# Optimization experiments

Hardware: AMD Instinct MI355X
Metric: run time of the kernel (lower is better)

Reference implementation:

```python
import jax, jax.numpy as jnp
import numpy as np

B, H, W, C, F, K = 64, 56, 56, 256, 256, 3


def _conv(x, w, padding):
    # NHWC input, HWIO kernel, stride 1
    return jax.lax.conv_general_dilated(
        x, w, window_strides=(1, 1), padding=padding,
        dimension_numbers=('NHWC', 'HWIO', 'NHWC'))


def setup_inputs() -> dict:
    key = jax.random.key(0)
    kx, kw = jax.random.split(key)
    x = jax.random.normal(kx, (B, H, W, C), dtype=jnp.float32)
    stdv = 1.0 / np.sqrt(K * K * C)  # matches build()'s init scale
    w = (jax.random.normal(kw, (K, K, C, F), dtype=jnp.float32) * stdv).astype(jnp.float32)
    return {"x": x, "w": w}


def reference(x, w):
    # fp16_grad forward: round-trip weights through fp16
    wq = w.astype(jnp.float16).astype(jnp.float32)
    # binarize_weight forward value: sign(clip(w, -1, 1))
    wb = jnp.sign(jnp.clip(wq, -1.0, 1.0))
    return _conv(x, wb, 'SAME')
```

## Files before the change

kernel.cpp:

```cpp
#include <hip/hip_runtime.h>
#include <hip/hip_bf16.h>
#include <hip/hip_fp16.h>

typedef __bf16 bf16x8 __attribute__((ext_vector_type(8)));
typedef float  f32x4  __attribute__((ext_vector_type(4)));

#define C_H 56
#define C_W 56
#define C_C 256
#define C_F 256
#define C_B 64
#define N_PIX (C_B * C_H * C_W)
#define WB_ELEMS (9 * C_C * C_F)
#define WB_BYTES (WB_ELEMS * 2)
#define ZBUF_BYTES 1024
#define XB_OFF (WB_BYTES + ZBUF_BYTES)
#define X_ELEMS (N_PIX * C_C)

#define GLOAD_LDS16(g, l)                                                   \
    __builtin_amdgcn_global_load_lds(                                        \
        (const __attribute__((address_space(1))) void*)(g),                  \
        (__attribute__((address_space(3))) void*)(l), 16, 0, 0)

__global__ void prep_w_kernel(const float* __restrict__ w, __bf16* __restrict__ wbT) {
    int idx = blockIdx.x * 256 + threadIdx.x;
    int f = idx & 255;
    int c = (idx >> 8) & 255;
    int s = idx >> 16;
    float wf = w[idx];
    float v = __half2float(__float2half(wf));
    float sgn = (v > 0.f) ? 1.f : ((v < 0.f) ? -1.f : 0.f);
    wbT[(s << 16) + (f << 8) + c] = (__bf16)sgn;
}

__global__ void zero_kernel(float* __restrict__ z) {
    z[threadIdx.x] = 0.f;
}

__global__ void prep_x_kernel(const float* __restrict__ x, __bf16* __restrict__ xb) {
    int i = blockIdx.x * 256 + threadIdx.x;
    const f32x4* p = reinterpret_cast<const f32x4*>(x) + (size_t)i * 2;
    f32x4 a = p[0], b = p[1];
    bf16x8 o;
    o[0] = (__bf16)a[0]; o[1] = (__bf16)a[1]; o[2] = (__bf16)a[2]; o[3] = (__bf16)a[3];
    o[4] = (__bf16)b[0]; o[5] = (__bf16)b[1]; o[6] = (__bf16)b[2]; o[7] = (__bf16)b[3];
    reinterpret_cast<bf16x8*>(xb)[i] = o;
}

__global__ __launch_bounds__(512, 2) void conv_mfma8_kernel(
    const char* __restrict__ xbp,
    const char* __restrict__ wbp,
    const char* __restrict__ zp,
    float* __restrict__ out) {

    __shared__ __align__(16) char sm[4][32768];

    const int nbid = (blockIdx.x & 7) * 98 + (blockIdx.x >> 3);
    const long m0 = (long)nbid * 256;

    const int tid  = threadIdx.x;
    const int lane = tid & 63;
    const int wave = tid >> 6;
    const int l15  = lane & 15;
    const int g4   = lane >> 4;
    const int wm   = wave >> 2;
    const int wn   = wave & 3;
    const int colr = ((g4 ^ ((l15 >> 1) & 3)) << 4);
    const int rdA = (wm * 128 + l15) * 64 + colr;
    const int rdB = 16384 + (wn * 64 + l15) * 64 + colr;

    const int r0 = tid >> 2;
    const int sw = ((tid & 3) ^ ((r0 >> 1) & 3)) << 4;
    const int p0 = (int)m0 + r0;
    const int p1 = p0 + 128;
    const int rem0 = p0 % 3136;
    const int rem1 = p1 % 3136;
    const int y0 = rem0 / 56, x0 = rem0 - (rem0 / 56) * 56;
    const int y1 = rem1 / 56, x1 = rem1 - (rem1 / 56) * 56;

    auto stage_half = [&](int kt, int abHalf) {
        int cc = (kt * 57) >> 9;
        int s  = kt - 9 * cc;
        char* L = &sm[kt & 3][0];
        size_t cb = (size_t)(cc << 6) + sw;
        if (abHalf == 0) {
            int s3 = (s * 171) >> 9;
            int dy = s3 - 1;
            int dx = s - 3 * s3 - 1;
            int doff = dy * 56 + dx;
            bool v0 = ((unsigned)(y0 + dy) < 56u) & ((unsigned)(x0 + dx) < 56u);
            bool v1 = ((unsigned)(y1 + dy) < 56u) & ((unsigned)(x1 + dx) < 56u);
            const char* a0 = v0 ? xbp + (size_t)(p0 + doff) * 512 + cb : zp + sw;
            const char* a1 = v1 ? xbp + (size_t)(p1 + doff) * 512 + cb : zp + sw;
            GLOAD_LDS16(a0, L + tid * 16);
            GLOAD_LDS16(a1, L + 8192 + tid * 16);
        } else {
            const char* b0 = wbp + (size_t)((s << 8) + r0) * 512 + cb;
            const char* b1 = wbp + (size_t)((s << 8) + r0 + 128) * 512 + cb;
            GLOAD_LDS16(b0, L + 16384 + tid * 16);
            GLOAD_LDS16(b1, L + 24576 + tid * 16);
        }
    };

    f32x4 acc[8][4];
#pragma unroll
    for (int i = 0; i < 8; ++i)
#pragma unroll
        for (int j = 0; j < 4; ++j)
            acc[i][j] = (f32x4){0.f, 0.f, 0.f, 0.f};

    bf16x8 Af[4], Bf[4];

#define VM8 asm volatile("s_waitcnt vmcnt(8)" ::: "memory")
#define VM4 asm volatile("s_waitcnt vmcnt(4)" ::: "memory")
#define VM0 asm volatile("s_waitcnt vmcnt(0)" ::: "memory")

#define PHASE(Q, H, DOSTAGE, TAILWAIT)                                      \
    {                                                                        \
        const char* Lb = &sm[(Q)][0];                                        \
        if ((H) == 0) {                                                      \
            _Pragma("unroll")                                                \
            for (int bj = 0; bj < 4; ++bj)                                   \
                Bf[bj] = *reinterpret_cast<const bf16x8*>(Lb + rdB + bj * 1024); \
        }                                                                    \
        _Pragma("unroll")                                                    \
        for (int ai = 0; ai < 4; ++ai)                                       \
            Af[ai] = *reinterpret_cast<const bf16x8*>(Lb + rdA + ((H) * 4 + ai) * 1024); \
        if (DOSTAGE) stage_half(kt + 3, (H));                                \
        __builtin_amdgcn_s_barrier();                                        \
        asm volatile("s_waitcnt lgkmcnt(0)" ::: "memory");                   \
        __builtin_amdgcn_sched_barrier(0);                                   \
        __builtin_amdgcn_s_setprio(1);                                       \
        _Pragma("unroll")                                                    \
        for (int ai = 0; ai < 4; ++ai)                                       \
            _Pragma("unroll")                                                \
            for (int bj = 0; bj < 4; ++bj)                                   \
                acc[(H) * 4 + ai][bj] = __builtin_amdgcn_mfma_f32_16x16x32_bf16( \
                    Af[ai], Bf[bj], acc[(H) * 4 + ai][bj], 0, 0, 0);         \
        __builtin_amdgcn_s_setprio(0);                                       \
        __builtin_amdgcn_sched_barrier(0);                                   \
        TAILWAIT;                                                            \
        __builtin_amdgcn_s_barrier();                                        \
    }

    stage_half(0, 0); stage_half(0, 1);
    stage_half(1, 0); stage_half(1, 1);
    stage_half(2, 0); stage_half(2, 1);
    VM8;
    __builtin_amdgcn_s_barrier();

    for (int it = 0; it < 17; ++it) {
        int kt;
        kt = it * 4 + 0; PHASE(0, 0, true, ); PHASE(0, 1, true, VM8);
        kt = it * 4 + 1; PHASE(1, 0, true, ); PHASE(1, 1, true, VM8);
        kt = it * 4 + 2; PHASE(2, 0, true, ); PHASE(2, 1, true, VM8);
        kt = it * 4 + 3; PHASE(3, 0, true, ); PHASE(3, 1, true, VM8);
    }
    { int kt = 68; PHASE(0, 0, true,  ); PHASE(0, 1, true,  VM8); }
    { int kt = 69; PHASE(1, 0, false, ); PHASE(1, 1, false, VM4); }
    { int kt = 70; PHASE(2, 0, false, ); PHASE(2, 1, false, VM0); }
    { int kt = 71; PHASE(3, 0, false, ); PHASE(3, 1, false, ); }

#undef PHASE

#pragma unroll
    for (int ai = 0; ai < 8; ++ai) {
#pragma unroll
        for (int j = 0; j < 4; ++j) {
            long row = m0 + wm * 128 + ai * 16 + g4 * 4 + j;
            float* op = out + row * C_F + wn * 64 + l15;
#pragma unroll
            for (int bj = 0; bj < 4; ++bj)
                op[bj * 16] = acc[ai][bj][j];
        }
    }
}

__global__ __launch_bounds__(256) void conv_fallback_kernel(
    const float* __restrict__ xf,
    const __bf16* __restrict__ wbT, const char* __restrict__ zbuf,
    float* __restrict__ out) {

    const int lane = threadIdx.x & 63;
    const int wave = threadIdx.x >> 6;
    const int l15  = lane & 15;
    const int g    = lane >> 4;
    const int goff = g * 8;
    const long m0  = (long)blockIdx.x * 64;
    const int fbase = wave * 64;

    int ry[4], rx[4];
    long rbase[4];
#pragma unroll
    for (int ai = 0; ai < 4; ++ai) {
        int rr = (int)m0 + ai * 16 + l15;
        int b = rr / 3136;
        int rem = rr - b * 3136;
        int yy2 = rem / 56;
        ry[ai] = yy2;
        rx[ai] = rem - yy2 * 56;
        rbase[ai] = (long)rr * C_C;
    }

    f32x4 acc[4][4];
#pragma unroll
    for (int i = 0; i < 4; ++i)
#pragma unroll
        for (int j = 0; j < 4; ++j)
            acc[i][j] = (f32x4){0.f, 0.f, 0.f, 0.f};

    for (int s = 0; s < 9; ++s) {
        const int dy = s / 3 - 1;
        const int dx = (s - (s / 3) * 3) - 1;
        const float* af[4];
#pragma unroll
        for (int ai = 0; ai < 4; ++ai) {
            bool v = ((unsigned)(ry[ai] + dy) < 56u) & ((unsigned)(rx[ai] + dx) < 56u);
            long off = rbase[ai] + (long)(dy * C_W + dx) * C_C + goff;
            af[ai] = v ? (xf + off) : ((const float*)zbuf + goff);
        }
        const __bf16* bp = wbT + ((size_t)(s * 256 + fbase + l15)) * C_C + goff;

#pragma unroll
        for (int cc = 0; cc < 8; ++cc) {
            const int c0 = cc * 32;
            bf16x8 A[4], Bf[4];
#pragma unroll
            for (int ai = 0; ai < 4; ++ai) {
                const f32x4* p = reinterpret_cast<const f32x4*>(af[ai] + c0);
                f32x4 u = p[0], w2 = p[1];
                bf16x8 t;
                t[0] = (__bf16)u[0]; t[1] = (__bf16)u[1]; t[2] = (__bf16)u[2]; t[3] = (__bf16)u[3];
                t[4] = (__bf16)w2[0]; t[5] = (__bf16)w2[1]; t[6] = (__bf16)w2[2]; t[7] = (__bf16)w2[3];
                A[ai] = t;
            }
#pragma unroll
            for (int bj = 0; bj < 4; ++bj)
                Bf[bj] = *reinterpret_cast<const bf16x8*>(bp + bj * 16 * C_C + c0);
#pragma unroll
            for (int ai = 0; ai < 4; ++ai)
#pragma unroll
                for (int bj = 0; bj < 4; ++bj)
                    acc[ai][bj] = __builtin_amdgcn_mfma_f32_16x16x32_bf16(A[ai], Bf[bj], acc[ai][bj], 0, 0, 0);
        }
    }

#pragma unroll
    for (int ai = 0; ai < 4; ++ai) {
#pragma unroll
        for (int j = 0; j < 4; ++j) {
            long row = m0 + ai * 16 + g * 4 + j;
            float* op = out + row * C_F + fbase + l15;
#pragma unroll
            for (int bj = 0; bj < 4; ++bj)
                op[bj * 16] = acc[ai][bj][j];
        }
    }
}

extern "C" void kernel_launch(void* const* d_in, const int* in_sizes, int n_in,
                              void* d_out, int out_size, void* d_ws, size_t ws_size,
                              hipStream_t stream) {
    const float* x = (const float*)d_in[0];
    const float* w = (const float*)d_in[1];
    float* out = (float*)d_out;

    char* ws = (char*)d_ws;
    __bf16* wbT = (__bf16*)ws;
    char* zbuf = ws + WB_BYTES;
    __bf16* xb = (__bf16*)(ws + XB_OFF);

    const bool prex = ws_size >= (size_t)XB_OFF + (size_t)X_ELEMS * 2;

    prep_w_kernel<<<WB_ELEMS / 256, 256, 0, stream>>>(w, wbT);
    zero_kernel<<<1, 256, 0, stream>>>((float*)zbuf);

    if (prex) {
        prep_x_kernel<<<X_ELEMS / 8 / 256, 256, 0, stream>>>(x, xb);
        conv_mfma8_kernel<<<N_PIX / 256, 512, 0, stream>>>(
            (const char*)xb, (const char*)wbT, zbuf, out);
    } else {
        conv_fallback_kernel<<<N_PIX / 64, 256, 0, stream>>>(x, wbT, zbuf, out);
    }
}
```

Before: 340.7 us.

## Shrink conv tile to 128x128 with 3-stage LDS ring and 256-thread blocks

Replaces the 256x256-tile, 512-thread, 4-buffer MFMA conv kernel with a 128x128 tile (split across M and F tiles), 256 threads, and a 3-deep LDS buffer ring with a single barrier per k-step. The goal is higher occupancy (3 blocks/CU), more blocks for load balance, and simpler synchronisation. The cost is lower arithmetic intensity per block: more global and LDS traffic per FLOP, since x tiles are now loaded twice (once per F half). It also drops the setprio and sched_barrier scheduling hints.

```diff
diff --git a/kernel.cpp b/kernel.cpp
--- a/kernel.cpp
+++ b/kernel.cpp
@@ -47,128 +47,110 @@
     reinterpret_cast<bf16x8*>(xb)[i] = o;
 }
 
-__global__ __launch_bounds__(512, 2) void conv_mfma8_kernel(
+__global__ __launch_bounds__(256, 3) void conv_p3_kernel(
     const char* __restrict__ xbp,
     const char* __restrict__ wbp,
     const char* __restrict__ zp,
     float* __restrict__ out) {
 
-    __shared__ __align__(16) char sm[4][32768];
-
-    const int nbid = (blockIdx.x & 7) * 98 + (blockIdx.x >> 3);
-    const long m0 = (long)nbid * 256;
+    __shared__ __align__(16) char sm[3][16384];
+
+    const int nbid = (blockIdx.x & 7) * 392 + (blockIdx.x >> 3);
+    const int mtile = nbid >> 1;
+    const int ftile = nbid & 1;
+    const long m0 = (long)mtile * 128;
+    const int fb0 = ftile * 128;
 
     const int tid  = threadIdx.x;
     const int lane = tid & 63;
     const int wave = tid >> 6;
     const int l15  = lane & 15;
     const int g4   = lane >> 4;
-    const int wm   = wave >> 2;
-    const int wn   = wave & 3;
+    const int wm   = wave >> 1;
+    const int wn   = wave & 1;
     const int colr = ((g4 ^ ((l15 >> 1) & 3)) << 4);
-    const int rdA = (wm * 128 + l15) * 64 + colr;
-    const int rdB = 16384 + (wn * 64 + l15) * 64 + colr;
+    const int rdA = (wm * 64 + l15) * 64 + colr;
+    const int rdB = 8192 + (wn * 64 + l15) * 64 + colr;
 
     const int r0 = tid >> 2;
-    const int sw = ((tid & 3) ^ ((r0 >> 1) & 3)) << 4;
+    const int sw = ((tid & 3) ^ ((tid >> 3) & 3)) << 4;
     const int p0 = (int)m0 + r0;
-    const int p1 = p0 + 128;
+    const int p1 = p0 + 64;
     const int rem0 = p0 % 3136;
     const int rem1 = p1 % 3136;
     const int y0 = rem0 / 56, x0 = rem0 - (rem0 / 56) * 56;
     const int y1 = rem1 / 56, x1 = rem1 - (rem1 / 56) * 56;
 
-    auto stage_half = [&](int kt, int abHalf) {
+    auto stage = [&](int kt, int sbuf) {
         int cc = (kt * 57) >> 9;
         int s  = kt - 9 * cc;
-        char* L = &sm[kt & 3][0];
+        int s3 = (s * 171) >> 9;
+        int dy = s3 - 1;
+        int dx = s - 3 * s3 - 1;
+        int doff = dy * 56 + dx;
         size_t cb = (size_t)(cc << 6) + sw;
-        if (abHalf == 0) {
-            int s3 = (s * 171) >> 9;
-            int dy = s3 - 1;
-            int dx = s - 3 * s3 - 1;
-            int doff = dy * 56 + dx;
-            bool v0 = ((unsigned)(y0 + dy) < 56u) & ((unsigned)(x0 + dx) < 56u);
-            bool v1 = ((unsigned)(y1 + dy) < 56u) & ((unsigned)(x1 + dx) < 56u);
-            const char* a0 = v0 ? xbp + (size_t)(p0 + doff) * 512 + cb : zp + sw;
-            const char* a1 = v1 ? xbp + (size_t)(p1 + doff) * 512 + cb : zp + sw;
-            GLOAD_LDS16(a0, L + tid * 16);
-            GLOAD_LDS16(a1, L + 8192 + tid * 16);
-        } else {
-            const char* b0 = wbp + (size_t)((s << 8) + r0) * 512 + cb;
-            const char* b1 = wbp + (size_t)((s << 8) + r0 + 128) * 512 + cb;
-            GLOAD_LDS16(b0, L + 16384 + tid * 16);
-            GLOAD_LDS16(b1, L + 24576 + tid * 16);
-        }
+        bool v0 = ((unsigned)(y0 + dy) < 56u) & ((unsigned)(x0 + dx) < 56u);
+        bool v1 = ((unsigned)(y1 + dy) < 56u) & ((unsigned)(x1 + dx) < 56u);
+        const char* a0 = v0 ? xbp + (size_t)(p0 + doff) * 512 + cb : zp + sw;
+        const char* a1 = v1 ? xbp + (size_t)(p1 + doff) * 512 + cb : zp + sw;
+        const char* b0 = wbp + (size_t)((s << 8) + fb0 + r0) * 512 + cb;
+        const char* b1 = b0 + (size_t)64 * 512;
+        char* L = &sm[sbuf][0];
+        GLOAD_LDS16(a0, L + tid * 16);
+        GLOAD_LDS16(a1, L + 4096 + tid * 16);
+        GLOAD_LDS16(b0, L + 8192 + tid * 16);
+        GLOAD_LDS16(b1, L + 12288 + tid * 16);
     };
 
-    f32x4 acc[8][4];
-#pragma unroll
-    for (int i = 0; i < 8; ++i)
+    f32x4 acc[4][4];
+#pragma unroll
+    for (int i = 0; i < 4; ++i)
 #pragma unroll
         for (int j = 0; j < 4; ++j)
             acc[i][j] = (f32x4){0.f, 0.f, 0.f, 0.f};
 
-    bf16x8 Af[4], Bf[4];
-
-#define VM8 asm volatile("s_waitcnt vmcnt(8)" ::: "memory")
-#define VM4 asm volatile("s_waitcnt vmcnt(4)" ::: "memory")
-#define VM0 asm volatile("s_waitcnt vmcnt(0)" ::: "memory")
-
-#define PHASE(Q, H, DOSTAGE, TAILWAIT)                                      \
+#define STEP(T, BUF, SBUF, DOSTAGE, WAITN)                                   \
     {                                                                        \
-        const char* Lb = &sm[(Q)][0];                                        \
-        if ((H) == 0) {                                                      \
-            _Pragma("unroll")                                                \
-            for (int bj = 0; bj < 4; ++bj)                                   \
-                Bf[bj] = *reinterpret_cast<const bf16x8*>(Lb + rdB + bj * 1024); \
-        }                                                                    \
+        asm volatile("s_waitcnt vmcnt(" WAITN ")" ::: "memory");             \
+        __builtin_amdgcn_s_barrier();                                        \
+        asm volatile("" ::: "memory");                                       \
+        const char* Lb = &sm[(BUF)][0];                                      \
+        bf16x8 Afr[4], Bfr[4];                                               \
         _Pragma("unroll")                                                    \
         for (int ai = 0; ai < 4; ++ai)                                       \
-            Af[ai] = *reinterpret_cast<const bf16x8*>(Lb + rdA + ((H) * 4 + ai) * 1024); \
-        if (DOSTAGE) stage_half(kt + 3, (H));                                \
-        __builtin_amdgcn_s_barrier();                                        \
-        asm volatile("s_waitcnt lgkmcnt(0)" ::: "memory");                   \
-        __builtin_amdgcn_sched_barrier(0);                                   \
-        __builtin_amdgcn_s_setprio(1);                                       \
+            Afr[ai] = *reinterpret_cast<const bf16x8*>(Lb + rdA + ai * 1024);\
+        _Pragma("unroll")                                                    \
+        for (int bj = 0; bj < 4; ++bj)                                       \
+            Bfr[bj] = *reinterpret_cast<const bf16x8*>(Lb + rdB + bj * 1024);\
+        if (DOSTAGE) stage((T) + 2, (SBUF));                                 \
         _Pragma("unroll")                                                    \
         for (int ai = 0; ai < 4; ++ai)                                       \
             _Pragma("unroll")                                                \
             for (int bj = 0; bj < 4; ++bj)                                   \
-                acc[(H) * 4 + ai][bj] = __builtin_amdgcn_mfma_f32_16x16x32_bf16( \
-                    Af[ai], Bf[bj], acc[(H) * 4 + ai][bj], 0, 0, 0);         \
-        __builtin_amdgcn_s_setprio(0);                                       \
-        __builtin_amdgcn_sched_barrier(0);                                   \
-        TAILWAIT;                                                            \
-        __builtin_amdgcn_s_barrier();                                        \
-    }
-
-    stage_half(0, 0); stage_half(0, 1);
-    stage_half(1, 0); stage_half(1, 1);
-    stage_half(2, 0); stage_half(2, 1);
-    VM8;
-    __builtin_amdgcn_s_barrier();
-
-    for (int it = 0; it < 17; ++it) {
-        int kt;
-        kt = it * 4 + 0; PHASE(0, 0, true, ); PHASE(0, 1, true, VM8);
-        kt = it * 4 + 1; PHASE(1, 0, true, ); PHASE(1, 1, true, VM8);
-        kt = it * 4 + 2; PHASE(2, 0, true, ); PHASE(2, 1, true, VM8);
-        kt = it * 4 + 3; PHASE(3, 0, true, ); PHASE(3, 1, true, VM8);
-    }
-    { int kt = 68; PHASE(0, 0, true,  ); PHASE(0, 1, true,  VM8); }
-    { int kt = 69; PHASE(1, 0, false, ); PHASE(1, 1, false, VM4); }
-    { int kt = 70; PHASE(2, 0, false, ); PHASE(2, 1, false, VM0); }
-    { int kt = 71; PHASE(3, 0, false, ); PHASE(3, 1, false, ); }
-
-#undef PHASE
-
-#pragma unroll
-    for (int ai = 0; ai < 8; ++ai) {
+                acc[ai][bj] = __builtin_amdgcn_mfma_f32_16x16x32_bf16(       \
+                    Afr[ai], Bfr[bj], acc[ai][bj], 0, 0, 0);                 \
+    }
+
+    stage(0, 0);
+    stage(1, 1);
+
+    for (int t = 0; t < 69; t += 3) {
+        STEP(t,     0, 2, true, "4");
+        STEP(t + 1, 1, 0, true, "4");
+        STEP(t + 2, 2, 1, true, "4");
+    }
+    STEP(69, 0, 2, true,  "4");
+    STEP(70, 1, 0, false, "4");
+    STEP(71, 2, 1, false, "0");
+
+#undef STEP
+
+#pragma unroll
+    for (int ai = 0; ai < 4; ++ai) {
 #pragma unroll
         for (int j = 0; j < 4; ++j) {
-            long row = m0 + wm * 128 + ai * 16 + g4 * 4 + j;
-            float* op = out + row * C_F + wn * 64 + l15;
+            long row = m0 + wm * 64 + ai * 16 + g4 * 4 + j;
+            float* op = out + row * C_F + fb0 + wn * 64 + l15;
 #pragma unroll
             for (int bj = 0; bj < 4; ++bj)
                 op[bj * 16] = acc[ai][bj][j];
@@ -277,7 +259,7 @@
 
     if (prex) {
         prep_x_kernel<<<X_ELEMS / 8 / 256, 256, 0, stream>>>(x, xb);
-        conv_mfma8_kernel<<<N_PIX / 256, 512, 0, stream>>>(
+        conv_p3_kernel<<<N_PIX / 128 * 2, 256, 0, stream>>>(
             (const char*)xb, (const char*)wbT, zbuf, out);
     } else {
         conv_fallback_kernel<<<N_PIX / 64, 256, 0, stream>>>(x, wbT, zbuf, out);
```

New measurement: 316.9 us. 1.08x faster.
